# Performance work log

Hardware: AMD Instinct MI355X
Metric: run time of the kernel (lower is better)

## Reference

```python
import jax, jax.numpy as jnp
import numpy as np

N_NODES = 50000

def mpnn_layer(x, edge_index, edge_weight, Wm, Wu, bu):
    # x: [N, Din]; Wm, Wu: [Dout, Din]; bu: [Dout]
    src, dst = edge_index[0], edge_index[1]
    m = x @ Wm.T                                   # [N, Dout] linear message
    msg = edge_weight[:, None] * m[src]            # gather + weight  [E, Dout]
    agg = jax.ops.segment_sum(msg, dst, num_segments=N_NODES)  # scatter-add
    return jnp.tanh(x @ Wu.T + bu + agg)

def setup_inputs() -> dict:
    key = jax.random.key(0)
    ks = jax.random.split(key, 16)
    N, E, D_IN, H, OUT = N_NODES, 800000, 128, 128, 32
    inp = {
        'x': jax.random.normal(ks[0], (N, D_IN), dtype=jnp.float32),
        'edge_index': jax.random.randint(ks[1], (2, E), 0, N, dtype=jnp.int64),
        'edge_weight': jax.random.uniform(ks[2], (E,), dtype=jnp.float32),
    }
    scale = 0.05
    dims = [D_IN, H, H]  # per-layer input dims
    for l in range(3):
        inp[f'Wm{l}'] = jax.random.normal(ks[3 + 3 * l], (H, dims[l]), dtype=jnp.float32) * scale
        inp[f'Wu{l}'] = jax.random.normal(ks[4 + 3 * l], (H, dims[l]), dtype=jnp.float32) * scale
        inp[f'bu{l}'] = jnp.zeros((H,), dtype=jnp.float32)
    inp['Wout'] = jax.random.normal(ks[13], (OUT, H), dtype=jnp.float32) * scale
    inp['bout'] = jnp.zeros((OUT,), dtype=jnp.float32)
    return inp

def reference(x, edge_index, edge_weight, Wm0, Wu0, bu0, Wm1, Wu1, bu1, Wm2, Wu2, bu2, Wout, bout):
    h = x
    for Wm, Wu, bu in ((Wm0, Wu0, bu0), (Wm1, Wu1, bu1), (Wm2, Wu2, bu2)):
        h = mpnn_layer(h, edge_index, edge_weight, Wm, Wu, bu)
    return h @ Wout.T + bout
```

## Files before the change

### kernel.cpp

```cpp
#include <hip/hip_runtime.h>
#include <hip/hip_bf16.h>
#include <cstddef>


typedef __attribute__((ext_vector_type(8))) short short8;
typedef __attribute__((ext_vector_type(4))) float f32x4;
typedef unsigned short ushort_t;
typedef unsigned int uint_t;

#define BSH 8
#define BSZ 256
#define CAPB 6144
#define TSTRIDE 16
#define EPB 2048

__device__ inline ushort_t f2bf(float f) {
    uint_t u = __float_as_uint(f);
    uint_t r = u + 0x7FFFu + ((u >> 16) & 1u);
    return (ushort_t)(r >> 16);
}
__device__ inline float bf_lo(uint_t u) { return __uint_as_float(u << 16); }
__device__ inline float bf_hi(uint_t u) { return __uint_as_float(u & 0xFFFF0000u); }
__device__ inline uint_t packbf(float a, float b) {
    return (uint_t)f2bf(a) | ((uint_t)f2bf(b) << 16);
}

__device__ inline float fast_tanh(float x) {
    float e = __builtin_amdgcn_exp2f(x * 2.8853900817779268f);
    return 1.f - 2.f * __builtin_amdgcn_rcpf(e + 1.f);
}

__device__ inline int get_dst(const int* __restrict__ ei, int e, int E, int f) {
    if (f) return ei[E + e];
    return ((const int2*)ei)[(size_t)E + e].x;
}
__device__ inline int get_src(const int* __restrict__ ei, int e, int E, int f) {
    if (f) return ei[e];
    return ((const int2*)ei)[e].x;
}

struct SetupArgs {
    const float* Wm0; const float* Wu0;
    const float* Wm1; const float* Wu1;
    const float* Wm2; const float* Wu2;
    const float* Wout;
    const float* x; const int* ei;
    ushort_t* wswz;
    ushort_t* woswz;
    ushort_t* xb;
    int* tails;
    int* flag;
    int N, E, TI;
    int ZT, WB, XB;
};
__global__ __launch_bounds__(256) void setup_kernel(SetupArgs a) {
    int bx = blockIdx.x, t = threadIdx.x;
    if (bx < a.ZT) {
        int i = bx * 256 + t;
        if (i < a.TI) a.tails[i] = 0;
        return;
    }
    bx -= a.ZT;
    if (bx == 0) {
        __shared__ int any;
        if (t == 0) any = 0;
        __syncthreads();
        int n = a.E < 2048 ? a.E : 2048;
        for (int i = t; i < n; i += 256)
            if (a.ei[2 * i + 1] != 0) any = 1;
        __syncthreads();
        if (t == 0) a.flag[0] = any;
        return;
    }
    bx -= 1;
    if (bx < a.WB) {
        int i = bx * 256 + t;
        if (i < 3 * 32768) {
            int l = i >> 15, r2 = i & 32767;
            int ct = r2 >> 12, ks = (r2 >> 9) & 7, lane = (r2 >> 3) & 63, j = r2 & 7;
            int col = ct * 16 + (lane & 15);
            int k = ks * 32 + (lane >> 4) * 8 + j;
            const float* Wm = l == 0 ? a.Wm0 : (l == 1 ? a.Wm1 : a.Wm2);
            const float* Wu = l == 0 ? a.Wu0 : (l == 1 ? a.Wu1 : a.Wu2);
            float v = k < 128 ? Wm[col * 128 + k] : Wu[col * 128 + (k - 128)];
            a.wswz[(size_t)l * 32768 + r2] = f2bf(v);
        } else if (i < 3 * 32768 + 4096) {
            int r2 = i - 3 * 32768;
            int ct = r2 >> 11, ks = (r2 >> 9) & 3, lane = (r2 >> 3) & 63, j = r2 & 7;
            int col = ct * 16 + (lane & 15);
            int k = ks * 32 + (lane >> 4) * 8 + j;
            a.woswz[r2] = f2bf(a.Wout[col * 128 + k]);
        }
        return;
    }
    bx -= a.WB;
    {
        int j = bx * 256 + t;
        if (j < a.N * 32) {
            float4 v = *(const float4*)(a.x + (size_t)j * 4);
            uint2 o;
            o.x = packbf(v.x, v.y);
            o.y = packbf(v.z, v.w);
            *(uint2*)(a.xb + (size_t)j * 4) = o;
        }
    }
}

__global__ __launch_bounds__(256) void bin_kernel(
    const int* __restrict__ ei, const float* __restrict__ ew,
    const int* __restrict__ flag, int* __restrict__ tails,
    uint2* __restrict__ staged, int E, int NB) {
    __shared__ uint2 ent[EPB];
    __shared__ int cnt[256], cur[256], runbase[256];
    const int tid = threadIdx.x;
    const int e0 = blockIdx.x * EPB;
    const int nE = (E - e0) < EPB ? (E - e0) : EPB;
    const int f = flag[0];
    cnt[tid] = 0;
    cur[tid] = 0;
    __syncthreads();
    for (int i = tid; i < nE; i += 256) {
        int e = e0 + i;
        int s = get_src(ei, e, E, f);
        int d = get_dst(ei, e, E, f);
        uint2 v;
        v.x = (uint_t)s | ((uint_t)f2bf(ew[e]) << 16);
        v.y = (uint_t)d;
        ent[i] = v;
        atomicAdd(&cnt[d >> BSH], 1);
    }
    __syncthreads();
    if (tid < NB) {
        int c = cnt[tid];
        runbase[tid] = c ? atomicAdd(&tails[tid * TSTRIDE], c) : 0;
    }
    __syncthreads();
    for (int i = tid; i < nE; i += 256) {
        uint2 v = ent[i];
        int d = (int)v.y;
        int b = d >> BSH;
        int lp = atomicAdd(&cur[b], 1);
        int gp = runbase[b] + lp;
        if (gp < CAPB) {
            uint2 o;
            o.x = v.x;
            o.y = (uint_t)(d & (BSZ - 1));
            staged[(size_t)b * CAPB + gp] = o;
        }
    }
}

__global__ __launch_bounds__(256) void place_kernel(
    const uint2* __restrict__ staged, const int* __restrict__ tails,
    int* __restrict__ cursor, uint_t* __restrict__ csr,
    int2* __restrict__ rowdeg, int N) {
    __shared__ int cnt[256], cur[256], excl[256], sm[256];
    __shared__ int baseSh;
    __shared__ uint_t outb[CAPB];
    const int b = blockIdx.x, tid = threadIdx.x;
    const int node0 = b << BSH;
    int tot = tails[b * TSTRIDE];
    tot = tot < CAPB ? tot : CAPB;
    cnt[tid] = 0;
    __syncthreads();
    const uint2* sp = staged + ((size_t)b * CAPB);
    for (int i = tid; i < tot; i += 256) atomicAdd(&cnt[sp[i].y], 1);
    __syncthreads();
    int c0 = cnt[tid];
    sm[tid] = c0;
    __syncthreads();
    for (int o = 1; o < 256; o <<= 1) {
        int v = tid >= o ? sm[tid - o] : 0;
        __syncthreads();
        sm[tid] += v;
        __syncthreads();
    }
    if (tid == 255) baseSh = atomicAdd(cursor, sm[255]);
    excl[tid] = sm[tid] - c0;
    cur[tid] = 0;
    __syncthreads();
    const int base = baseSh;
    for (int i = tid; i < tot; i += 256) {
        uint2 e = sp[i];
        int pos = excl[e.y] + atomicAdd(&cur[e.y], 1);
        outb[pos] = e.x;
    }
    __syncthreads();
    for (int i = tid; i < tot; i += 256) csr[base + i] = outb[i];
    if (node0 + tid < N) {
        int2 be;
        be.x = base + excl[tid];
        be.y = base + excl[tid] + c0;
        rowdeg[node0 + tid] = be;
    }
}

__global__ __launch_bounds__(256) void aggregate_g(
    const uint_t* __restrict__ csr, const int2* __restrict__ rowdeg,
    const ushort_t* __restrict__ h, ushort_t* __restrict__ g, int N) {
    int node = (blockIdx.x * 256 + threadIdx.x) >> 6;
    if (node >= N) return;
    int lane = threadIdx.x & 63;
    int slot = lane >> 3, f8 = lane & 7;
    int2 be = rowdeg[node];
    int beg = be.x, end = be.y;
    float s[16];
#pragma unroll
    for (int k = 0; k < 16; ++k) s[k] = 0.f;
    for (int j = beg + slot; j < end; j += 8) {
        uint_t p = csr[j];
        float w = bf_hi(p);
        const ushort_t* row = h + (size_t)(p & 0xFFFFu) * 128 + f8 * 16;
        uint4 v0 = *(const uint4*)(row);
        uint4 v1 = *(const uint4*)(row + 8);
        s[0] += w * bf_lo(v0.x);  s[1] += w * bf_hi(v0.x);
        s[2] += w * bf_lo(v0.y);  s[3] += w * bf_hi(v0.y);
        s[4] += w * bf_lo(v0.z);  s[5] += w * bf_hi(v0.z);
        s[6] += w * bf_lo(v0.w);  s[7] += w * bf_hi(v0.w);
        s[8] += w * bf_lo(v1.x);  s[9] += w * bf_hi(v1.x);
        s[10] += w * bf_lo(v1.y); s[11] += w * bf_hi(v1.y);
        s[12] += w * bf_lo(v1.z); s[13] += w * bf_hi(v1.z);
        s[14] += w * bf_lo(v1.w); s[15] += w * bf_hi(v1.w);
    }
#pragma unroll
    for (int k = 0; k < 16; ++k) s[k] += __shfl_xor(s[k], 8, 64);
#pragma unroll
    for (int k = 0; k < 16; ++k) s[k] += __shfl_xor(s[k], 16, 64);
#pragma unroll
    for (int k = 0; k < 16; ++k) s[k] += __shfl_xor(s[k], 32, 64);
    if (slot == 0) {
        uint4 o0, o1;
        o0.x = packbf(s[0], s[1]);   o0.y = packbf(s[2], s[3]);
        o0.z = packbf(s[4], s[5]);   o0.w = packbf(s[6], s[7]);
        o1.x = packbf(s[8], s[9]);   o1.y = packbf(s[10], s[11]);
        o1.z = packbf(s[12], s[13]); o1.w = packbf(s[14], s[15]);
        ushort_t* gp = g + (size_t)node * 128 + f8 * 16;
        *(uint4*)(gp) = o0;
        *(uint4*)(gp + 8) = o1;
    }
}

__global__ __launch_bounds__(256) void fused_gemm(
    const ushort_t* __restrict__ G, const ushort_t* __restrict__ H,
    const ushort_t* __restrict__ Wswz, const float* __restrict__ bias,
    ushort_t* __restrict__ Hout, int N) {
    __shared__ ushort_t wl[32768];
    const int tid = threadIdx.x;
    const int lane = tid & 63;
    const int row0 = blockIdx.x * 64 + (tid >> 6) * 16;
    const int m = lane & 15, kg = lane >> 4;

    const ushort_t* ag = G + (size_t)(row0 + m) * 128 + kg * 8;
    const ushort_t* ah = H + (size_t)(row0 + m) * 128 + kg * 8;

    short8 a[8];
#pragma unroll
    for (int ks = 0; ks < 4; ++ks) a[ks] = *(const short8*)(ag + ks * 32);
#pragma unroll
    for (int ks = 0; ks < 4; ++ks) a[4 + ks] = *(const short8*)(ah + ks * 32);

#pragma unroll
    for (int i = 0; i < 16; ++i) {
        uint4 v = *(const uint4*)(Wswz + ((size_t)i * 256 + tid) * 8);
        *(uint4*)(wl + (i * 256 + tid) * 8) = v;
    }
    __syncthreads();

    f32x4 acc[8];
#pragma unroll
    for (int ct = 0; ct < 8; ++ct) acc[ct] = (f32x4){0.f, 0.f, 0.f, 0.f};

#pragma unroll
    for (int ksp = 0; ksp < 8; ++ksp) {
#pragma unroll
        for (int ct = 0; ct < 8; ++ct) {
            short8 b = *(const short8*)(wl + ((ct * 8 + ksp) * 64 + lane) * 8);
            acc[ct] = __builtin_amdgcn_mfma_f32_16x16x32_bf16(a[ksp], b, acc[ct], 0, 0, 0);
        }
    }
    const int colL = lane & 15, rq = lane >> 4;
#pragma unroll
    for (int ct = 0; ct < 8; ++ct) {
        int col = ct * 16 + colL;
        float bv = bias[col];
#pragma unroll
        for (int reg = 0; reg < 4; ++reg) {
            int gr = row0 + rq * 4 + reg;
            if (gr < N) Hout[(size_t)gr * 128 + col] = f2bf(fast_tanh(acc[ct][reg] + bv));
        }
    }
}

__global__ __launch_bounds__(256) void mfma_gemm_out(
    const ushort_t* __restrict__ H, const ushort_t* __restrict__ Wswz,
    const float* __restrict__ bias, float* __restrict__ C, int N) {
    const int tid = threadIdx.x;
    const int lane = tid & 63;
    const int row0 = blockIdx.x * 64 + (tid >> 6) * 16;
    const int m = lane & 15;
    const ushort_t* ah = H + (size_t)(row0 + m) * 128 + (lane >> 4) * 8;

    short8 a[4], b[8];
#pragma unroll
    for (int ks = 0; ks < 4; ++ks) a[ks] = *(const short8*)(ah + ks * 32);
#pragma unroll
    for (int ks = 0; ks < 4; ++ks) {
#pragma unroll
        for (int ct = 0; ct < 2; ++ct)
            b[ks * 2 + ct] = *(const short8*)(Wswz + ((ct * 4 + ks) * 64 + lane) * 8);
    }

    f32x4 acc[2];
#pragma unroll
    for (int ct = 0; ct < 2; ++ct) acc[ct] = (f32x4){0.f, 0.f, 0.f, 0.f};
#pragma unroll
    for (int ks = 0; ks < 4; ++ks) {
#pragma unroll
        for (int ct = 0; ct < 2; ++ct)
            acc[ct] = __builtin_amdgcn_mfma_f32_16x16x32_bf16(a[ks], b[ks * 2 + ct], acc[ct], 0, 0, 0);
    }
    const int colL = lane & 15, rq = lane >> 4;
#pragma unroll
    for (int ct = 0; ct < 2; ++ct) {
        int col = ct * 16 + colL;
        float bv = bias[col];
#pragma unroll
        for (int reg = 0; reg < 4; ++reg) {
            int gr = row0 + rq * 4 + reg;
            if (gr < N) C[(size_t)gr * 32 + col] = acc[ct][reg] + bv;
        }
    }
}

extern "C" void kernel_launch(void* const* d_in, const int* in_sizes, int n_in,
                              void* d_out, int out_size, void* d_ws, size_t ws_size,
                              hipStream_t stream) {
    const float* x   = (const float*)d_in[0];
    const int* ei    = (const int*)d_in[1];
    const float* ew  = (const float*)d_in[2];
    const float* Wm[3] = {(const float*)d_in[3], (const float*)d_in[6], (const float*)d_in[9]};
    const float* Wu[3] = {(const float*)d_in[4], (const float*)d_in[7], (const float*)d_in[10]};
    const float* bu[3] = {(const float*)d_in[5], (const float*)d_in[8], (const float*)d_in[11]};
    const float* Wout = (const float*)d_in[12];
    const float* bout = (const float*)d_in[13];
    float* out = (float*)d_out;

    const int N = in_sizes[0] / 128;
    const int E = in_sizes[2];
    const size_t NPAD = 50048;
    const int NB = (N + BSZ - 1) / BSZ;
    const int TI = NB * TSTRIDE + 16;

    ushort_t* xb    = (ushort_t*)d_ws;
    ushort_t* hA    = xb + NPAD * 128;
    ushort_t* hB    = hA + NPAD * 128;
    ushort_t* gbuf  = hB + NPAD * 128;
    ushort_t* wswz  = gbuf + NPAD * 128;
    ushort_t* woswz = wswz + 3 * 32768;
    int* flag       = (int*)(woswz + 4096);
    int* tails      = flag + 1;
    int* cursor     = tails + NB * TSTRIDE;
    int* endp       = tails + TI;
    int2* rowdeg    = (int2*)(((uintptr_t)endp + 7) & ~(uintptr_t)7);
    uint2* staged   = (uint2*)(rowdeg + N + 8);
    uint_t* csr     = (uint_t*)(staged + (size_t)NB * CAPB);
    (void)ws_size;

    const int ZT = (TI + 255) / 256;
    const int WB = (3 * 32768 + 4096 + 255) / 256;
    const int XB = (N * 32 + 255) / 256;
    const int gB = (E + EPB - 1) / EPB;
    const int gG = (N + 63) / 64;
    const int gA = (N + 3) / 4;
    const int gO = (N + 63) / 64;

    SetupArgs sa;
    sa.Wm0 = Wm[0]; sa.Wu0 = Wu[0];
    sa.Wm1 = Wm[1]; sa.Wu1 = Wu[1];
    sa.Wm2 = Wm[2]; sa.Wu2 = Wu[2];
    sa.Wout = Wout; sa.x = x; sa.ei = ei;
    sa.wswz = wswz; sa.woswz = woswz; sa.xb = xb;
    sa.tails = tails; sa.flag = flag;
    sa.N = N; sa.E = E; sa.TI = TI;
    sa.ZT = ZT; sa.WB = WB; sa.XB = XB;
    setup_kernel<<<ZT + 1 + WB + XB, 256, 0, stream>>>(sa);

    bin_kernel<<<gB, 256, 0, stream>>>(ei, ew, flag, tails, staged, E, NB);
    place_kernel<<<NB, 256, 0, stream>>>(staged, tails, cursor, csr, rowdeg, N);

    const ushort_t* hin[3] = {xb, hA, hB};
    ushort_t* hout[3] = {hA, hB, hA};
    for (int l = 0; l < 3; ++l) {
        aggregate_g<<<gA, 256, 0, stream>>>(csr, rowdeg, hin[l], gbuf, N);
        fused_gemm<<<gG, 256, 0, stream>>>(gbuf, hin[l], wswz + (size_t)l * 32768,
                                           bu[l], hout[l], N);
    }
    mfma_gemm_out<<<gO, 256, 0, stream>>>(hA, woswz, bout, out, N);
}
```

Before: 284.4 us.

## Unroll aggregation gather by two and split fused GEMM columns across waves

The aggregation loop now processes two edges per iteration so more independent gathers are in flight. The fused GEMM drops its 64KB LDS weight staging. Each wave now holds the B fragments for two of the eight column tiles in registers and loops over all four 16-row blocks of the tile. This removes LDS capacity pressure and the block barrier, raising occupancy (launch bounds 4). The cost is that each wave reloads A rows for every row block (4x A traffic per wave, served from cache) and uses more registers.

```diff
diff --git a/kernel.cpp b/kernel.cpp
--- a/kernel.cpp
+++ b/kernel.cpp
@@ -207,7 +207,35 @@
     float s[16];
 #pragma unroll
     for (int k = 0; k < 16; ++k) s[k] = 0.f;
-    for (int j = beg + slot; j < end; j += 8) {
+    int j = beg + slot;
+    for (; j + 8 < end; j += 16) {
+        uint_t p0 = csr[j];
+        uint_t p1 = csr[j + 8];
+        float w0 = bf_hi(p0), w1 = bf_hi(p1);
+        const ushort_t* r0 = h + (size_t)(p0 & 0xFFFFu) * 128 + f8 * 16;
+        const ushort_t* r1 = h + (size_t)(p1 & 0xFFFFu) * 128 + f8 * 16;
+        uint4 v0 = *(const uint4*)(r0);
+        uint4 v1 = *(const uint4*)(r0 + 8);
+        uint4 u0 = *(const uint4*)(r1);
+        uint4 u1 = *(const uint4*)(r1 + 8);
+        s[0] += w0 * bf_lo(v0.x);  s[1] += w0 * bf_hi(v0.x);
+        s[2] += w0 * bf_lo(v0.y);  s[3] += w0 * bf_hi(v0.y);
+        s[4] += w0 * bf_lo(v0.z);  s[5] += w0 * bf_hi(v0.z);
+        s[6] += w0 * bf_lo(v0.w);  s[7] += w0 * bf_hi(v0.w);
+        s[8] += w0 * bf_lo(v1.x);  s[9] += w0 * bf_hi(v1.x);
+        s[10] += w0 * bf_lo(v1.y); s[11] += w0 * bf_hi(v1.y);
+        s[12] += w0 * bf_lo(v1.z); s[13] += w0 * bf_hi(v1.z);
+        s[14] += w0 * bf_lo(v1.w); s[15] += w0 * bf_hi(v1.w);
+        s[0] += w1 * bf_lo(u0.x);  s[1] += w1 * bf_hi(u0.x);
+        s[2] += w1 * bf_lo(u0.y);  s[3] += w1 * bf_hi(u0.y);
+        s[4] += w1 * bf_lo(u0.z);  s[5] += w1 * bf_hi(u0.z);
+        s[6] += w1 * bf_lo(u0.w);  s[7] += w1 * bf_hi(u0.w);
+        s[8] += w1 * bf_lo(u1.x);  s[9] += w1 * bf_hi(u1.x);
+        s[10] += w1 * bf_lo(u1.y); s[11] += w1 * bf_hi(u1.y);
+        s[12] += w1 * bf_lo(u1.z); s[13] += w1 * bf_hi(u1.z);
+        s[14] += w1 * bf_lo(u1.w); s[15] += w1 * bf_hi(u1.w);
+    }
+    if (j < end) {
         uint_t p = csr[j];
         float w = bf_hi(p);
         const ushort_t* row = h + (size_t)(p & 0xFFFFu) * 128 + f8 * 16;
@@ -240,53 +268,52 @@
     }
 }
 
-__global__ __launch_bounds__(256) void fused_gemm(
+__global__ __launch_bounds__(256, 4) void fused_gemm(
     const ushort_t* __restrict__ G, const ushort_t* __restrict__ H,
     const ushort_t* __restrict__ Wswz, const float* __restrict__ bias,
     ushort_t* __restrict__ Hout, int N) {
-    __shared__ ushort_t wl[32768];
     const int tid = threadIdx.x;
     const int lane = tid & 63;
-    const int row0 = blockIdx.x * 64 + (tid >> 6) * 16;
+    const int wave = tid >> 6;
+    const int row0 = blockIdx.x * 64;
     const int m = lane & 15, kg = lane >> 4;
-
-    const ushort_t* ag = G + (size_t)(row0 + m) * 128 + kg * 8;
-    const ushort_t* ah = H + (size_t)(row0 + m) * 128 + kg * 8;
-
-    short8 a[8];
-#pragma unroll
-    for (int ks = 0; ks < 4; ++ks) a[ks] = *(const short8*)(ag + ks * 32);
-#pragma unroll
-    for (int ks = 0; ks < 4; ++ks) a[4 + ks] = *(const short8*)(ah + ks * 32);
-
-#pragma unroll
-    for (int i = 0; i < 16; ++i) {
-        uint4 v = *(const uint4*)(Wswz + ((size_t)i * 256 + tid) * 8);
-        *(uint4*)(wl + (i * 256 + tid) * 8) = v;
-    }
-    __syncthreads();
-
-    f32x4 acc[8];
-#pragma unroll
-    for (int ct = 0; ct < 8; ++ct) acc[ct] = (f32x4){0.f, 0.f, 0.f, 0.f};
-
-#pragma unroll
-    for (int ksp = 0; ksp < 8; ++ksp) {
-#pragma unroll
-        for (int ct = 0; ct < 8; ++ct) {
-            short8 b = *(const short8*)(wl + ((ct * 8 + ksp) * 64 + lane) * 8);
-            acc[ct] = __builtin_amdgcn_mfma_f32_16x16x32_bf16(a[ksp], b, acc[ct], 0, 0, 0);
-        }
-    }
     const int colL = lane & 15, rq = lane >> 4;
-#pragma unroll
-    for (int ct = 0; ct < 8; ++ct) {
-        int col = ct * 16 + colL;
-        float bv = bias[col];
+
+    short8 b[2][8];
+#pragma unroll
+    for (int c = 0; c < 2; ++c)
+#pragma unroll
+        for (int ksp = 0; ksp < 8; ++ksp)
+            b[c][ksp] = *(const short8*)(Wswz + (((2 * wave + c) * 8 + ksp) * 64 + lane) * 8);
+
+    const float bv0 = bias[(2 * wave) * 16 + colL];
+    const float bv1 = bias[(2 * wave + 1) * 16 + colL];
+
+#pragma unroll
+    for (int gblk = 0; gblk < 4; ++gblk) {
+        const int r = row0 + gblk * 16 + m;
+        const ushort_t* ag = G + (size_t)r * 128 + kg * 8;
+        const ushort_t* ah = H + (size_t)r * 128 + kg * 8;
+        short8 a[8];
+#pragma unroll
+        for (int ks = 0; ks < 4; ++ks) a[ks] = *(const short8*)(ag + ks * 32);
+#pragma unroll
+        for (int ks = 0; ks < 4; ++ks) a[4 + ks] = *(const short8*)(ah + ks * 32);
+
+        f32x4 acc0 = (f32x4){0.f, 0.f, 0.f, 0.f};
+        f32x4 acc1 = (f32x4){0.f, 0.f, 0.f, 0.f};
+#pragma unroll
+        for (int ksp = 0; ksp < 8; ++ksp) {
+            acc0 = __builtin_amdgcn_mfma_f32_16x16x32_bf16(a[ksp], b[0][ksp], acc0, 0, 0, 0);
+            acc1 = __builtin_amdgcn_mfma_f32_16x16x32_bf16(a[ksp], b[1][ksp], acc1, 0, 0, 0);
+        }
 #pragma unroll
         for (int reg = 0; reg < 4; ++reg) {
-            int gr = row0 + rq * 4 + reg;
-            if (gr < N) Hout[(size_t)gr * 128 + col] = f2bf(fast_tanh(acc[ct][reg] + bv));
+            int gr = row0 + gblk * 16 + rq * 4 + reg;
+            if (gr < N) {
+                Hout[(size_t)gr * 128 + (2 * wave) * 16 + colL] = f2bf(fast_tanh(acc0[reg] + bv0));
+                Hout[(size_t)gr * 128 + (2 * wave + 1) * 16 + colL] = f2bf(fast_tanh(acc1[reg] + bv1));
+            }
         }
     }
 }
```

Result: no change. 283.2 us (-0.4%).
